# Optimization experiments

Measured on AMD Instinct MI355X. Metric: run time of the kernel, lower is better.

Reference implementation:

```python
import jax, jax.numpy as jnp
import numpy as np

SEQ, BATCH, INPT, HIDDEN = 2048, 512, 64, 128

def setup_inputs() -> dict:
    key = jax.random.key(0)
    ks = jax.random.split(key, 7)
    s = 1.0 / np.sqrt(HIDDEN)
    return {
        "xs": jax.random.normal(ks[0], (SEQ, BATCH, INPT), dtype=jnp.float32),
        "W_ih": jax.random.uniform(ks[1], (HIDDEN, INPT), minval=-s, maxval=s, dtype=jnp.float32),
        "W_hh": jax.random.uniform(ks[2], (HIDDEN, HIDDEN), minval=-s, maxval=s, dtype=jnp.float32),
        "b_ih": jax.random.uniform(ks[3], (HIDDEN,), minval=-s, maxval=s, dtype=jnp.float32),
        "b_hh": jax.random.uniform(ks[4], (HIDDEN,), minval=-s, maxval=s, dtype=jnp.float32),
        "W_out": jax.random.uniform(ks[5], (1, HIDDEN), minval=-s, maxval=s, dtype=jnp.float32),
        "b_out": jax.random.uniform(ks[6], (1,), minval=-s, maxval=s, dtype=jnp.float32),
    }

def reference(xs, W_ih, W_hh, b_ih, b_hh, W_out, b_out):
    # RNNCell: h' = tanh(x @ W_ih^T + b_ih + h @ W_hh^T + b_hh); h0 = 0
    batch = xs.shape[1]
    h0 = jnp.zeros((batch, W_hh.shape[0]), dtype=xs.dtype)

    def step(h, x):
        h_new = jnp.tanh(x @ W_ih.T + b_ih + h @ W_hh.T + b_hh)
        return h_new, None

    h_final, _ = jax.lax.scan(step, h0, xs)
    return h_final @ W_out.T + b_out  # [batch, 1]
```

## Files before the change

### kernel.cpp

```cpp
#include <hip/hip_runtime.h>
#include <hip/hip_bf16.h>

#define SEQ   2048
#define BATCH 512
#define INPT  64
#define HID   128
#define KTOT  192
#define NSL   8
#define KSH   24
#define NOUT  4

typedef _Float16 half2_t __attribute__((ext_vector_type(2)));
typedef _Float16 half4_t __attribute__((ext_vector_type(4)));
typedef float    float4_t __attribute__((ext_vector_type(4)));

#if defined(__has_builtin)
#if __has_builtin(__builtin_amdgcn_fdot2)
#define HAVE_FDOT2 1
#endif
#endif

__device__ __forceinline__ float fdot2f(half2_t a, half2_t b, float c) {
#ifdef HAVE_FDOT2
    return __builtin_amdgcn_fdot2(a, b, c, false);
#else
    return fmaf((float)a[0], (float)b[0], fmaf((float)a[1], (float)b[1], c));
#endif
}

template <int CTRL>
__device__ __forceinline__ float dpp_xor_add(float v) {
    int x = __builtin_amdgcn_update_dpp(0, __builtin_bit_cast(int, v), CTRL, 0xF, 0xF, true);
    return v + __builtin_bit_cast(float, x);
}
__device__ __forceinline__ float swz_xor4_add(float v) {
    int x = __builtin_amdgcn_ds_swizzle(__builtin_bit_cast(int, v), 0x101F);
    return v + __builtin_bit_cast(float, x);
}

__device__ __forceinline__ float tanh_fast(float a) {
    float e = __expf(2.0f * a);
    float r = __builtin_amdgcn_rcpf(e + 1.0f);
    return fmaf(-2.0f, r, 1.0f);
}

__global__ __launch_bounds__(256, 2) void rnn_kernel(
    const float* __restrict__ xs,   const float* __restrict__ W_ih,
    const float* __restrict__ W_hh, const float* __restrict__ b_ih,
    const float* __restrict__ b_hh, const float* __restrict__ W_out,
    const float* __restrict__ b_out, float* __restrict__ out)
{
    const int row = blockIdx.x;
    const int tid = threadIdx.x;
    const int s   = tid & (NSL - 1);
    const int jg  = tid >> 3;
    const int k0  = s * KSH;

    __shared__ alignas(16) _Float16 F[2][KTOT];

    half2_t w[NOUT][KSH / 2];
    float bsum[NOUT];
    #pragma unroll
    for (int c = 0; c < NOUT; ++c) {
        const int r = jg * NOUT + c;
        bsum[c] = b_ih[r] + b_hh[r];
        #pragma unroll
        for (int p = 0; p < KSH / 2; ++p) {
            int k = k0 + 2 * p;
            float w0 = (k     < 64) ? W_ih[r * INPT + k]     : W_hh[r * HID + (k - 64)];
            float w1 = (k + 1 < 64) ? W_ih[r * INPT + k + 1] : W_hh[r * HID + (k + 1 - 64)];
            half2_t hw; hw[0] = (_Float16)w0; hw[1] = (_Float16)w1;
            w[c][p] = hw;
        }
    }

    const float*  xrow    = xs + (size_t)row * INPT;
    const size_t  tstride = (size_t)BATCH * INPT;

    if (tid < 64) ((int*)&F[0][64])[tid] = 0;
    float4_t P0, P1;
    if (tid < 16) {
        float4_t x0 = *((const float4_t*)(xrow + 0 * tstride) + tid);
        half4_t h4; h4[0] = (_Float16)x0[0]; h4[1] = (_Float16)x0[1];
        h4[2] = (_Float16)x0[2]; h4[3] = (_Float16)x0[3];
        *(half4_t*)&F[0][4 * tid] = h4;
        P1 = *((const float4_t*)(xrow + 1 * tstride) + tid);
        P0 = *((const float4_t*)(xrow + 2 * tstride) + tid);
    }
    __syncthreads();

    auto step = [&](int t, int cur, int nxt, float4_t& P) {
        union { int4 i4[3]; half2_t h2[12]; } u;
        const int4* src = (const int4*)&F[cur][k0];
        u.i4[0] = src[0]; u.i4[1] = src[1]; u.i4[2] = src[2];

        float a0 = 0.0f, a1 = 0.0f, a2 = 0.0f, a3 = 0.0f;
        #pragma unroll
        for (int p = 0; p < 12; ++p) {
            a0 = fdot2f(u.h2[p], w[0][p], a0);
            a1 = fdot2f(u.h2[p], w[1][p], a1);
            a2 = fdot2f(u.h2[p], w[2][p], a2);
            a3 = fdot2f(u.h2[p], w[3][p], a3);
        }
        a0 = dpp_xor_add<0xB1>(a0); a0 = dpp_xor_add<0x4E>(a0); a0 = swz_xor4_add(a0);
        a1 = dpp_xor_add<0xB1>(a1); a1 = dpp_xor_add<0x4E>(a1); a1 = swz_xor4_add(a1);
        a2 = dpp_xor_add<0xB1>(a2); a2 = dpp_xor_add<0x4E>(a2); a2 = swz_xor4_add(a2);
        a3 = dpp_xor_add<0xB1>(a3); a3 = dpp_xor_add<0x4E>(a3); a3 = swz_xor4_add(a3);

        float va = (s == 0) ? a0 + bsum[0] : a2 + bsum[2];
        float vb = (s == 0) ? a1 + bsum[1] : a3 + bsum[3];
        if ((s & 3) == 0) {
            float ha = tanh_fast(va);
            float hb = tanh_fast(vb);
            int off = 64 + jg * 4 + ((s >> 1) & 2);
            half2_t hh; hh[0] = (_Float16)ha; hh[1] = (_Float16)hb;
            *(half2_t*)&F[nxt][off] = hh;
        }
        if (tid < 16) {
            half4_t h4; h4[0] = (_Float16)P[0]; h4[1] = (_Float16)P[1];
            h4[2] = (_Float16)P[2]; h4[3] = (_Float16)P[3];
            *(half4_t*)&F[nxt][4 * tid] = h4;
            if (t + 3 < SEQ)
                P = *((const float4_t*)(xrow + (size_t)(t + 3) * tstride) + tid);
        }
        __syncthreads();
    };

    for (int t2 = 0; t2 < SEQ; t2 += 2) {
        step(t2,     0, 1, P1);
        step(t2 + 1, 1, 0, P0);
    }

    if (tid < 64) {
        float p = (float)F[0][64 + tid]      * W_out[tid]
                + (float)F[0][64 + 64 + tid] * W_out[64 + tid];
        p += __shfl_xor(p, 1);  p += __shfl_xor(p, 2);  p += __shfl_xor(p, 4);
        p += __shfl_xor(p, 8);  p += __shfl_xor(p, 16); p += __shfl_xor(p, 32);
        if (tid == 0) out[row] = p + b_out[0];
    }
}

extern "C" void kernel_launch(void* const* d_in, const int* in_sizes, int n_in,
                              void* d_out, int out_size, void* d_ws, size_t ws_size,
                              hipStream_t stream) {
    const float* xs    = (const float*)d_in[0];
    const float* W_ih  = (const float*)d_in[1];
    const float* W_hh  = (const float*)d_in[2];
    const float* b_ih  = (const float*)d_in[3];
    const float* b_hh  = (const float*)d_in[4];
    const float* W_out = (const float*)d_in[5];
    const float* b_out = (const float*)d_in[6];
    float* out = (float*)d_out;

    rnn_kernel<<<dim3(BATCH), dim3(256), 0, stream>>>(
        xs, W_ih, W_hh, b_ih, b_hh, W_out, b_out, out);
}
```

Measured before the change: 1.229 ms.

## Rewrite RNN recurrence with MFMA over 16-row batch tiles per block

Replaces the one-batch-row-per-block fdot2 kernel with blocks that each handle 16 batch rows. Each step computes h@W^T and x@W^T with 16x16x32 f16 MFMA instructions, with 8 waves each owning 16 hidden outputs. Input chunks of 16 timesteps are staged in LDS through double buffering and register prefetch, which cuts per-step global loads and cross-lane reductions. In exchange only 32 blocks are launched, so most of the GPU sits idle, and each step's serial latency is now bound by the MFMA chain plus a 512-thread barrier.

After: 1.191 ms. -3.1%, faster.

```diff
diff --git a/kernel.cpp b/kernel.cpp
--- a/kernel.cpp
+++ b/kernel.cpp
@@ -1,42 +1,18 @@
 #include <hip/hip_runtime.h>
-#include <hip/hip_bf16.h>
 
 #define SEQ   2048
 #define BATCH 512
 #define INPT  64
 #define HID   128
-#define KTOT  192
-#define NSL   8
-#define KSH   24
-#define NOUT  4
+#define ROWS  16
+#define NBLK  (BATCH/ROWS)
+#define CHUNK 16
+#define XSTR  72
+#define HSTR  136
 
-typedef _Float16 half2_t __attribute__((ext_vector_type(2)));
-typedef _Float16 half4_t __attribute__((ext_vector_type(4)));
-typedef float    float4_t __attribute__((ext_vector_type(4)));
-
-#if defined(__has_builtin)
-#if __has_builtin(__builtin_amdgcn_fdot2)
-#define HAVE_FDOT2 1
-#endif
-#endif
-
-__device__ __forceinline__ float fdot2f(half2_t a, half2_t b, float c) {
-#ifdef HAVE_FDOT2
-    return __builtin_amdgcn_fdot2(a, b, c, false);
-#else
-    return fmaf((float)a[0], (float)b[0], fmaf((float)a[1], (float)b[1], c));
-#endif
-}
-
-template <int CTRL>
-__device__ __forceinline__ float dpp_xor_add(float v) {
-    int x = __builtin_amdgcn_update_dpp(0, __builtin_bit_cast(int, v), CTRL, 0xF, 0xF, true);
-    return v + __builtin_bit_cast(float, x);
-}
-__device__ __forceinline__ float swz_xor4_add(float v) {
-    int x = __builtin_amdgcn_ds_swizzle(__builtin_bit_cast(int, v), 0x101F);
-    return v + __builtin_bit_cast(float, x);
-}
+typedef _Float16 f16x8 __attribute__((ext_vector_type(8)));
+typedef _Float16 f16x4 __attribute__((ext_vector_type(4)));
+typedef float    f32x4 __attribute__((ext_vector_type(4)));
 
 __device__ __forceinline__ float tanh_fast(float a) {
     float e = __expf(2.0f * a);
@@ -44,99 +20,126 @@
     return fmaf(-2.0f, r, 1.0f);
 }
 
-__global__ __launch_bounds__(256, 2) void rnn_kernel(
+__global__ __launch_bounds__(512) void rnn_mfma(
     const float* __restrict__ xs,   const float* __restrict__ W_ih,
     const float* __restrict__ W_hh, const float* __restrict__ b_ih,
     const float* __restrict__ b_hh, const float* __restrict__ W_out,
     const float* __restrict__ b_out, float* __restrict__ out)
 {
-    const int row = blockIdx.x;
-    const int tid = threadIdx.x;
-    const int s   = tid & (NSL - 1);
-    const int jg  = tid >> 3;
-    const int k0  = s * KSH;
+    const int tid  = threadIdx.x;
+    const int lane = tid & 63;
+    const int wv   = tid >> 6;
+    const int n0   = wv * 16;
+    const int ml   = lane & 15;
+    const int kq   = lane >> 4;
+    const int r0   = blockIdx.x * ROWS;
 
-    __shared__ alignas(16) _Float16 F[2][KTOT];
+    __shared__ _Float16 xb[2][CHUNK * ROWS * XSTR];
+    __shared__ _Float16 hb[2][ROWS * HSTR];
 
-    half2_t w[NOUT][KSH / 2];
-    float bsum[NOUT];
-    #pragma unroll
-    for (int c = 0; c < NOUT; ++c) {
-        const int r = jg * NOUT + c;
-        bsum[c] = b_ih[r] + b_hh[r];
+    f16x8 bf[6];
+    {
+        const int n = n0 + ml;
         #pragma unroll
-        for (int p = 0; p < KSH / 2; ++p) {
-            int k = k0 + 2 * p;
-            float w0 = (k     < 64) ? W_ih[r * INPT + k]     : W_hh[r * HID + (k - 64)];
-            float w1 = (k + 1 < 64) ? W_ih[r * INPT + k + 1] : W_hh[r * HID + (k + 1 - 64)];
-            half2_t hw; hw[0] = (_Float16)w0; hw[1] = (_Float16)w1;
-            w[c][p] = hw;
+        for (int kt = 0; kt < 6; ++kt) {
+            f16x8 v;
+            #pragma unroll
+            for (int j = 0; j < 8; ++j) {
+                int k = kt * 32 + kq * 8 + j;
+                float wval = (k < 64) ? W_ih[n * INPT + k] : W_hh[n * HID + (k - 64)];
+                v[j] = (_Float16)wval;
+            }
+            bf[kt] = v;
         }
     }
+    const float bias = b_ih[n0 + ml] + b_hh[n0 + ml];
 
-    const float*  xrow    = xs + (size_t)row * INPT;
-    const size_t  tstride = (size_t)BATCH * INPT;
+    for (int i = tid; i < ROWS * 64; i += 512) {
+        int m = i >> 6, w = i & 63;
+        ((int*)&hb[0][m * HSTR])[w] = 0;
+    }
 
-    if (tid < 64) ((int*)&F[0][64])[tid] = 0;
-    float4_t P0, P1;
-    if (tid < 16) {
-        float4_t x0 = *((const float4_t*)(xrow + 0 * tstride) + tid);
-        half4_t h4; h4[0] = (_Float16)x0[0]; h4[1] = (_Float16)x0[1];
-        h4[2] = (_Float16)x0[2]; h4[3] = (_Float16)x0[3];
-        *(half4_t*)&F[0][4 * tid] = h4;
-        P1 = *((const float4_t*)(xrow + 1 * tstride) + tid);
-        P0 = *((const float4_t*)(xrow + 2 * tstride) + tid);
+    const int sts  = tid >> 5;
+    const int srem = tid & 31;
+    f32x4 st[8];
+    #pragma unroll
+    for (int j = 0; j < 8; ++j) {
+        int flat = srem + 32 * j, m = flat >> 4, e4 = flat & 15;
+        st[j] = *(const f32x4*)&xs[((size_t)sts * BATCH + r0 + m) * INPT + e4 * 4];
+    }
+    #pragma unroll
+    for (int j = 0; j < 8; ++j) {
+        int flat = srem + 32 * j, m = flat >> 4, e4 = flat & 15;
+        f16x4 o; o[0] = (_Float16)st[j][0]; o[1] = (_Float16)st[j][1];
+                 o[2] = (_Float16)st[j][2]; o[3] = (_Float16)st[j][3];
+        *(f16x4*)&xb[0][(sts * ROWS + m) * XSTR + e4 * 4] = o;
     }
     __syncthreads();
 
-    auto step = [&](int t, int cur, int nxt, float4_t& P) {
-        union { int4 i4[3]; half2_t h2[12]; } u;
-        const int4* src = (const int4*)&F[cur][k0];
-        u.i4[0] = src[0]; u.i4[1] = src[1]; u.i4[2] = src[2];
+    for (int t = 0; t < SEQ; ++t) {
+        const int kc  = t & (CHUNK - 1);
+        const int cb  = (t >> 4) & 1;
+        const int hbi = t & 1;
 
-        float a0 = 0.0f, a1 = 0.0f, a2 = 0.0f, a3 = 0.0f;
+        const _Float16* xr = &xb[cb][(kc * ROWS + ml) * XSTR + kq * 8];
+        f16x8 a0 = *(const f16x8*)(xr);
+        f16x8 a1 = *(const f16x8*)(xr + 32);
+        const _Float16* hr = &hb[hbi][ml * HSTR + kq * 8];
+        f16x8 a2 = *(const f16x8*)(hr);
+        f16x8 a3 = *(const f16x8*)(hr + 32);
+        f16x8 a4 = *(const f16x8*)(hr + 64);
+        f16x8 a5 = *(const f16x8*)(hr + 96);
+
+        if (kc == 0 && t + CHUNK < SEQ) {
+            #pragma unroll
+            for (int j = 0; j < 8; ++j) {
+                int flat = srem + 32 * j, m = flat >> 4, e4 = flat & 15;
+                st[j] = *(const f32x4*)&xs[((size_t)(t + CHUNK + sts) * BATCH + r0 + m) * INPT + e4 * 4];
+            }
+        }
+
+        f32x4 acc1 = {0.f, 0.f, 0.f, 0.f}, acc2 = {0.f, 0.f, 0.f, 0.f};
+        acc1 = __builtin_amdgcn_mfma_f32_16x16x32_f16(a0, bf[0], acc1, 0, 0, 0);
+        acc2 = __builtin_amdgcn_mfma_f32_16x16x32_f16(a1, bf[1], acc2, 0, 0, 0);
+        acc1 = __builtin_amdgcn_mfma_f32_16x16x32_f16(a2, bf[2], acc1, 0, 0, 0);
+        acc2 = __builtin_amdgcn_mfma_f32_16x16x32_f16(a3, bf[3], acc2, 0, 0, 0);
+        acc1 = __builtin_amdgcn_mfma_f32_16x16x32_f16(a4, bf[4], acc1, 0, 0, 0);
+        acc2 = __builtin_amdgcn_mfma_f32_16x16x32_f16(a5, bf[5], acc2, 0, 0, 0);
+
+        _Float16* hw = &hb[hbi ^ 1][0];
         #pragma unroll
-        for (int p = 0; p < 12; ++p) {
-            a0 = fdot2f(u.h2[p], w[0][p], a0);
-            a1 = fdot2f(u.h2[p], w[1][p], a1);
-            a2 = fdot2f(u.h2[p], w[2][p], a2);
-            a3 = fdot2f(u.h2[p], w[3][p], a3);
+        for (int q = 0; q < 4; ++q) {
+            float v  = acc1[q] + acc2[q] + bias;
+            float hv = tanh_fast(v);
+            hw[(kq * 4 + q) * HSTR + n0 + ml] = (_Float16)hv;
         }
-        a0 = dpp_xor_add<0xB1>(a0); a0 = dpp_xor_add<0x4E>(a0); a0 = swz_xor4_add(a0);
-        a1 = dpp_xor_add<0xB1>(a1); a1 = dpp_xor_add<0x4E>(a1); a1 = swz_xor4_add(a1);
-        a2 = dpp_xor_add<0xB1>(a2); a2 = dpp_xor_add<0x4E>(a2); a2 = swz_xor4_add(a2);
-        a3 = dpp_xor_add<0xB1>(a3); a3 = dpp_xor_add<0x4E>(a3); a3 = swz_xor4_add(a3);
 
-        float va = (s == 0) ? a0 + bsum[0] : a2 + bsum[2];
-        float vb = (s == 0) ? a1 + bsum[1] : a3 + bsum[3];
-        if ((s & 3) == 0) {
-            float ha = tanh_fast(va);
-            float hb = tanh_fast(vb);
-            int off = 64 + jg * 4 + ((s >> 1) & 2);
-            half2_t hh; hh[0] = (_Float16)ha; hh[1] = (_Float16)hb;
-            *(half2_t*)&F[nxt][off] = hh;
+        if (kc == 8 && t + 8 < SEQ) {
+            #pragma unroll
+            for (int j = 0; j < 8; ++j) {
+                int flat = srem + 32 * j, m = flat >> 4, e4 = flat & 15;
+                f16x4 o; o[0] = (_Float16)st[j][0]; o[1] = (_Float16)st[j][1];
+                         o[2] = (_Float16)st[j][2]; o[3] = (_Float16)st[j][3];
+                *(f16x4*)&xb[cb ^ 1][(sts * ROWS + m) * XSTR + e4 * 4] = o;
+            }
         }
-        if (tid < 16) {
-            half4_t h4; h4[0] = (_Float16)P[0]; h4[1] = (_Float16)P[1];
-            h4[2] = (_Float16)P[2]; h4[3] = (_Float16)P[3];
-            *(half4_t*)&F[nxt][4 * tid] = h4;
-            if (t + 3 < SEQ)
-                P = *((const float4_t*)(xrow + (size_t)(t + 3) * tstride) + tid);
-        }
-        __syncthreads();
-    };
 
-    for (int t2 = 0; t2 < SEQ; t2 += 2) {
-        step(t2,     0, 1, P1);
-        step(t2 + 1, 1, 0, P0);
+        asm volatile("s_waitcnt lgkmcnt(0)" ::: "memory");
+        __builtin_amdgcn_s_barrier();
+        __builtin_amdgcn_sched_barrier(0);
     }
 
-    if (tid < 64) {
-        float p = (float)F[0][64 + tid]      * W_out[tid]
-                + (float)F[0][64 + 64 + tid] * W_out[64 + tid];
-        p += __shfl_xor(p, 1);  p += __shfl_xor(p, 2);  p += __shfl_xor(p, 4);
-        p += __shfl_xor(p, 8);  p += __shfl_xor(p, 16); p += __shfl_xor(p, 32);
-        if (tid == 0) out[row] = p + b_out[0];
+    {
+        const int m = tid >> 5, c = tid & 31;
+        float p = 0.f;
+        #pragma unroll
+        for (int j = 0; j < 4; ++j) {
+            int n = c * 4 + j;
+            p += (float)hb[0][m * HSTR + n] * W_out[n];
+        }
+        p += __shfl_xor(p, 1); p += __shfl_xor(p, 2); p += __shfl_xor(p, 4);
+        p += __shfl_xor(p, 8); p += __shfl_xor(p, 16);
+        if (c == 0) out[r0 + m] = p + b_out[0];
     }
 }
 
@@ -152,6 +155,6 @@
     const float* b_out = (const float*)d_in[6];
     float* out = (float*)d_out;
 
-    rnn_kernel<<<dim3(BATCH), dim3(256), 0, stream>>>(
+    rnn_mfma<<<dim3(NBLK), dim3(512), 0, stream>>>(
         xs, W_ih, W_hh, b_ih, b_hh, W_out, b_out, out);
 }
```
